# Kernel tuning notes

Hardware: AMD Instinct MI355X
Metric: run time of the kernel (lower is better)

Reference implementation:

```python
import jax, jax.numpy as jnp
import numpy as np

B, L, M = 32768, 128, 1024  # batch, latent_size, num_basis_function


def setup_inputs() -> dict:
    key = jax.random.key(0)
    k1, k2, k3 = jax.random.split(key, 3)
    u_lat = jax.random.normal(k1, (B, L), dtype=jnp.float32)
    centres = jax.random.normal(k2, (M, L), dtype=jnp.float32)      # RBF centres (torch init: N(0,1))
    log_sigmas = jnp.zeros((M,), dtype=jnp.float32)                  # RBF log bandwidths (torch init: 0)
    lin1_w = jax.random.normal(k3, (M,), dtype=jnp.float32) / np.float32(np.sqrt(M))  # Linear(M,1,bias=False)
    return {"u_lat": u_lat, "centres": centres, "log_sigmas": log_sigmas, "lin1_w": lin1_w}


def _V_batch(u, centres, log_sigmas, lin1_w):
    """Potential V(h) = ELU(w . multiquadric(||h-c||/sigma)) + 0.5*||h||^2, per row. Returns [B]."""
    u_sq = jnp.sum(u * u, axis=-1)                                   # [B]
    c_sq = jnp.sum(centres * centres, axis=-1)                       # [M]
    # ||h - c||^2 via norm expansion: avoids [B, M, L] intermediate
    sq_dist = jnp.maximum(u_sq[:, None] + c_sq[None, :] - 2.0 * (u @ centres.T), 0.0)  # [B, M]
    d = jnp.sqrt(sq_dist) / jnp.exp(log_sigmas)[None, :]             # [B, M]
    phi = jnp.sqrt(1.0 + d * d)                                      # multiquadric kernel
    e = jax.nn.elu(phi @ lin1_w)                                     # [B]
    return e + 0.5 * u_sq


def reference(u_lat, centres, log_sigmas, lin1_w):
    # LEBNN.forward: f_lat = dV/dh evaluated per sample (vmap(jacrev) in torch).
    # Each entry of _V_batch depends only on its own row of u_lat, so
    # grad of the summed potential gives the per-sample Jacobian rows exactly.
    grad_fn = jax.grad(lambda u: jnp.sum(_V_batch(u, centres, log_sigmas, lin1_w)))
    return grad_fn(u_lat)  # [B, L]
```

## Files before the change

### kernel.cpp

```cpp
#include <hip/hip_runtime.h>
#include <math.h>

#define B_N 32768
#define L_N 128
#define M_N 1024
#define NT 512
#define TB 64
#define TM 64
#define NCHUNK (M_N / TM)

typedef __bf16 v8bf __attribute__((ext_vector_type(8)));
typedef __bf16 v4bf __attribute__((ext_vector_type(4)));
typedef float  v4f  __attribute__((ext_vector_type(4)));

#define MFMA(a, b, c) __builtin_amdgcn_mfma_f32_16x16x32_bf16(a, b, c, 0, 0, 0)

#define US  136
#define CNS 136

__device__ inline v8bf pack8(float4 a, float4 b) {
    v8bf v;
    v[0] = (__bf16)a.x; v[1] = (__bf16)a.y; v[2] = (__bf16)a.z; v[3] = (__bf16)a.w;
    v[4] = (__bf16)b.x; v[5] = (__bf16)b.y; v[6] = (__bf16)b.z; v[7] = (__bf16)b.w;
    return v;
}

__global__ void lebnn_precompute(const float* __restrict__ centres,
                                 const float* __restrict__ log_sigmas,
                                 const float* __restrict__ lin_w,
                                 float4* __restrict__ cpack) {
    int m = blockIdx.x * blockDim.x + threadIdx.x;
    if (m >= M_N) return;
    const float4* row = (const float4*)(centres + (size_t)m * L_N);
    float s = 0.f;
#pragma unroll
    for (int i = 0; i < L_N / 4; ++i) {
        float4 v = row[i];
        s += v.x * v.x + v.y * v.y + v.z * v.z + v.w * v.w;
    }
    float4 p;
    p.x = s;
    p.y = expf(-2.f * log_sigmas[m]);
    p.z = lin_w[m];
    p.w = 0.f;
    cpack[m] = p;
}

__global__ void lebnn_transpose(const float* __restrict__ centres,
                                __bf16* __restrict__ cT) {
    __shared__ __bf16 tile[64 * 72];
    const int m0 = blockIdx.x * 64;
    const int l0 = blockIdx.y * 64;
    const int row = threadIdx.x >> 2;
    const int seg = threadIdx.x & 3;
    const float* src = centres + (size_t)(m0 + row) * L_N + l0 + seg * 16;
    float4 a0 = *(const float4*)(src);
    float4 a1 = *(const float4*)(src + 4);
    float4 a2 = *(const float4*)(src + 8);
    float4 a3 = *(const float4*)(src + 12);
    *(v8bf*)&tile[row * 72 + seg * 16]     = pack8(a0, a1);
    *(v8bf*)&tile[row * 72 + seg * 16 + 8] = pack8(a2, a3);
    __syncthreads();
    v8bf o0, o1;
#pragma unroll
    for (int i = 0; i < 8; ++i) o0[i] = tile[(seg * 16 + i) * 72 + row];
#pragma unroll
    for (int i = 0; i < 8; ++i) o1[i] = tile[(seg * 16 + 8 + i) * 72 + row];
    __bf16* dst = cT + (size_t)(l0 + row) * M_N + m0 + seg * 16;
    *(v8bf*)(dst)     = o0;
    *(v8bf*)(dst + 8) = o1;
}

__global__ __launch_bounds__(NT) void lebnn_phase1(
    const float* __restrict__ u, const float* __restrict__ centres,
    const float4* __restrict__ cpack, __bf16* __restrict__ qg,
    float* __restrict__ gg, float* __restrict__ rsg)
{
    __shared__ __bf16 u_bf[64 * US];
    __shared__ __bf16 c_n[64 * CNS];
    __shared__ float usq_s[64];
    __shared__ float upart[64 * 9];
    __shared__ float sred[288];
    __shared__ float rred[288];

    const int tid  = threadIdx.x;
    const int w    = tid >> 6;
    const int lane = tid & 63;
    const int l15  = lane & 15;
    const int l4   = lane >> 4;
    const int bh   = w >> 2;
    const int mq   = w & 3;
    const int b0   = blockIdx.x * TB;

    {
        int row = tid >> 3, seg = tid & 7;
        const float* up = u + (size_t)(b0 + row) * L_N + seg * 16;
        float4 a0 = *(const float4*)(up);
        float4 a1 = *(const float4*)(up + 4);
        float4 a2 = *(const float4*)(up + 8);
        float4 a3 = *(const float4*)(up + 12);
        float ps = a0.x*a0.x + a0.y*a0.y + a0.z*a0.z + a0.w*a0.w
                 + a1.x*a1.x + a1.y*a1.y + a1.z*a1.z + a1.w*a1.w
                 + a2.x*a2.x + a2.y*a2.y + a2.z*a2.z + a2.w*a2.w
                 + a3.x*a3.x + a3.y*a3.y + a3.z*a3.z + a3.w*a3.w;
        *(v8bf*)&u_bf[row * US + seg * 16]     = pack8(a0, a1);
        *(v8bf*)&u_bf[row * US + seg * 16 + 8] = pack8(a2, a3);
        upart[row * 9 + seg] = ps;
    }
    __syncthreads();
    if (tid < TB) {
        float s = 0.f;
#pragma unroll
        for (int i = 0; i < 8; ++i) s += upart[tid * 9 + i];
        usq_s[tid] = s;
    }
    __syncthreads();

    v8bf uf[2][4];
#pragma unroll
    for (int bt = 0; bt < 2; ++bt)
#pragma unroll
        for (int kk = 0; kk < 4; ++kk)
            uf[bt][kk] = *(v8bf*)&u_bf[(bh*32 + bt*16 + l15) * US + kk*32 + l4*8];

    float usq_r[2][4];
#pragma unroll
    for (int bt = 0; bt < 2; ++bt)
#pragma unroll
        for (int r = 0; r < 4; ++r)
            usq_r[bt][r] = usq_s[bh*32 + bt*16 + l4*4 + r];

    float s_p[2][4] = {{0.f,0.f,0.f,0.f},{0.f,0.f,0.f,0.f}};
    float r_p[2][4] = {{0.f,0.f,0.f,0.f},{0.f,0.f,0.f,0.f}};

    const int rp = tid >> 4;
    const int cg = tid & 15;

    for (int mt = 0; mt < NCHUNK; ++mt) {
        const int m0 = mt * TM;
        __syncthreads();
        {
            const float* cp0 = centres + (size_t)(m0 + 2*rp) * L_N + cg * 8;
            float4 r0a = *(const float4*)(cp0);
            float4 r0b = *(const float4*)(cp0 + 4);
            float4 r1a = *(const float4*)(cp0 + L_N);
            float4 r1b = *(const float4*)(cp0 + L_N + 4);
            *(v8bf*)&c_n[(2*rp)     * CNS + cg*8] = pack8(r0a, r0b);
            *(v8bf*)&c_n[(2*rp + 1) * CNS + cg*8] = pack8(r1a, r1b);
        }
        float4 cpv = cpack[m0 + mq*16 + l15];
        __syncthreads();

        v4f dot[2];
        dot[0] = (v4f){0.f,0.f,0.f,0.f};
        dot[1] = (v4f){0.f,0.f,0.f,0.f};
#pragma unroll
        for (int kk = 0; kk < 4; ++kk) {
            v8bf bfr = *(v8bf*)&c_n[(mq*16 + l15) * CNS + kk*32 + l4*8];
            dot[0] = MFMA(uf[0][kk], bfr, dot[0]);
            dot[1] = MFMA(uf[1][kk], bfr, dot[1]);
        }

        v8bf qv8;
        const float wq = cpv.z * cpv.y;
#pragma unroll
        for (int bt = 0; bt < 2; ++bt) {
#pragma unroll
            for (int r = 0; r < 4; ++r) {
                float dv  = dot[bt][r];
                float raw = fmaf(-2.f, dv, usq_r[bt][r] + cpv.x);
                float x   = fmaf(fmaxf(raw, 0.f), cpv.y, 1.f);
                float ri  = rsqrtf(x);
                s_p[bt][r] = fmaf(cpv.z, x * ri, s_p[bt][r]);
                float qv  = (raw > 0.f) ? wq * ri : 0.f;
                r_p[bt][r] += qv;
                qv8[bt*4 + r] = (__bf16)qv;
            }
        }
        *(v8bf*)(qg + ((size_t)blockIdx.x * NCHUNK + mt) * (NT * 8) + tid * 8) = qv8;
    }

#pragma unroll
    for (int bt = 0; bt < 2; ++bt)
#pragma unroll
        for (int r = 0; r < 4; ++r) {
#pragma unroll
            for (int msk = 1; msk < 16; msk <<= 1) {
                s_p[bt][r] += __shfl_xor(s_p[bt][r], msk, 64);
                r_p[bt][r] += __shfl_xor(r_p[bt][r], msk, 64);
            }
        }
    if (l15 == 0) {
#pragma unroll
        for (int bt = 0; bt < 2; ++bt)
#pragma unroll
            for (int r = 0; r < 4; ++r) {
                sred[w*36 + bt*16 + l4*4 + r] = s_p[bt][r];
                rred[w*36 + bt*16 + l4*4 + r] = r_p[bt][r];
            }
    }
    __syncthreads();

    if (tid < TB) {
        int bhh = tid >> 5, rowr = tid & 31;
        float s = 0.f, R = 0.f;
#pragma unroll
        for (int i = 0; i < 4; ++i) {
            s += sred[(bhh*4 + i)*36 + rowr];
            R += rred[(bhh*4 + i)*36 + rowr];
        }
        float g = (s > 0.f) ? 1.f : expf(s);
        gg[b0 + tid]  = g;
        rsg[b0 + tid] = fmaf(g, R, 1.f);
    }
}

__global__ __launch_bounds__(NT) void lebnn_gemm2(
    const float* __restrict__ u, const __bf16* __restrict__ qg,
    const __bf16* __restrict__ cT, const float* __restrict__ gg,
    const float* __restrict__ rsg, float* __restrict__ out)
{
    __shared__ __bf16 qt[64 * 72];
    __shared__ __bf16 ct[128 * 72];

    const int tid  = threadIdx.x;
    const int w    = tid >> 6;
    const int lane = tid & 63;
    const int l15  = lane & 15;
    const int l4   = lane >> 4;
    const int bh   = w >> 2;
    const int lq   = w & 3;
    const int bb0  = blockIdx.x * 64;

    v4f acc[2][2];
#pragma unroll
    for (int bt = 0; bt < 2; ++bt)
#pragma unroll
        for (int lt = 0; lt < 2; ++lt)
            acc[bt][lt] = (v4f){0.f, 0.f, 0.f, 0.f};

    for (int mt = 0; mt < NCHUNK; ++mt) {
        const int m0 = mt * TM;
        __syncthreads();
        {
            v8bf qv = *(const v8bf*)(qg + ((size_t)blockIdx.x * NCHUNK + mt) * (NT * 8) + tid * 8);
#pragma unroll
            for (int bt = 0; bt < 2; ++bt)
#pragma unroll
                for (int r = 0; r < 4; ++r)
                    qt[(bh*32 + bt*16 + l4*4 + r) * 72 + lq*16 + l15] = qv[bt*4 + r];
        }
        {
            int lr = tid >> 2, sg = tid & 3;
            const __bf16* src = cT + (size_t)lr * M_N + m0 + sg * 16;
            *(v8bf*)&ct[lr * 72 + sg * 16]     = *(const v8bf*)(src);
            *(v8bf*)&ct[lr * 72 + sg * 16 + 8] = *(const v8bf*)(src + 8);
        }
        __syncthreads();

#pragma unroll
        for (int kk = 0; kk < 2; ++kk) {
            v8bf qa0 = *(v8bf*)&qt[(bh*32 +  0 + l15) * 72 + kk*32 + l4*8];
            v8bf qa1 = *(v8bf*)&qt[(bh*32 + 16 + l15) * 72 + kk*32 + l4*8];
#pragma unroll
            for (int lt = 0; lt < 2; ++lt) {
                v8bf cb = *(v8bf*)&ct[(lq*32 + lt*16 + l15) * 72 + kk*32 + l4*8];
                acc[0][lt] = MFMA(qa0, cb, acc[0][lt]);
                acc[1][lt] = MFMA(qa1, cb, acc[1][lt]);
            }
        }
    }

    float gv[2][4], rv[2][4];
#pragma unroll
    for (int bt = 0; bt < 2; ++bt)
#pragma unroll
        for (int r = 0; r < 4; ++r) {
            int b = bb0 + bh*32 + bt*16 + l4*4 + r;
            gv[bt][r] = gg[b];
            rv[bt][r] = rsg[b];
        }
#pragma unroll
    for (int bt = 0; bt < 2; ++bt)
#pragma unroll
        for (int lt = 0; lt < 2; ++lt)
#pragma unroll
            for (int r = 0; r < 4; ++r) {
                size_t idx = (size_t)(bb0 + bh*32 + bt*16 + l4*4 + r) * L_N
                           + lq*32 + lt*16 + l15;
                out[idx] = fmaf(u[idx], rv[bt][r], -gv[bt][r] * acc[bt][lt][r]);
            }
}

#define CFS 68
#define OFF_UBF   0
#define OFF_CN    17408
#define OFF_CFL   34816
#define OFF_USQ   52224
#define OFF_UPART 52480
#define OFF_SRED  54784
#define OFF_RRED  55936
#define OFF_G     57088
#define OFF_RS    57344
#define SMEM_BYTES 57600

__global__ __launch_bounds__(NT) void lebnn_fallback(
    const float* __restrict__ u, const float* __restrict__ centres,
    const float4* __restrict__ cpack, float* __restrict__ out)
{
    extern __shared__ char smem[];
    __bf16* u_bf = (__bf16*)(smem + OFF_UBF);
    __bf16* c_n  = (__bf16*)(smem + OFF_CN);
    float*  cfl  = (float*)(smem + OFF_CFL);
    float* usq_s = (float*)(smem + OFF_USQ);
    float* upart = (float*)(smem + OFF_UPART);
    float* sred  = (float*)(smem + OFF_SRED);
    float* rred  = (float*)(smem + OFF_RRED);
    float* gsh   = (float*)(smem + OFF_G);
    float* rssh  = (float*)(smem + OFF_RS);

    const int tid  = threadIdx.x;
    const int w    = tid >> 6;
    const int lane = tid & 63;
    const int l15  = lane & 15;
    const int l4   = lane >> 4;
    const int bh   = w >> 2;
    const int mq   = w & 3;
    const int tx   = tid & 15;
    const int ty   = tid >> 4;
    const int b0   = blockIdx.x * TB;

    {
        int row = tid >> 3, seg = tid & 7;
        const float* up = u + (size_t)(b0 + row) * L_N + seg * 16;
        float4 a0 = *(const float4*)(up);
        float4 a1 = *(const float4*)(up + 4);
        float4 a2 = *(const float4*)(up + 8);
        float4 a3 = *(const float4*)(up + 12);
        float ps = a0.x*a0.x + a0.y*a0.y + a0.z*a0.z + a0.w*a0.w
                 + a1.x*a1.x + a1.y*a1.y + a1.z*a1.z + a1.w*a1.w
                 + a2.x*a2.x + a2.y*a2.y + a2.z*a2.z + a2.w*a2.w
                 + a3.x*a3.x + a3.y*a3.y + a3.z*a3.z + a3.w*a3.w;
        *(v8bf*)&u_bf[row * US + seg * 16]     = pack8(a0, a1);
        *(v8bf*)&u_bf[row * US + seg * 16 + 8] = pack8(a2, a3);
        upart[row * 9 + seg] = ps;
    }
    __syncthreads();
    if (tid < TB) {
        float s = 0.f;
#pragma unroll
        for (int i = 0; i < 8; ++i) s += upart[tid * 9 + i];
        usq_s[tid] = s;
    }
    __syncthreads();

    v8bf uf[2][4];
#pragma unroll
    for (int bt = 0; bt < 2; ++bt)
#pragma unroll
        for (int kk = 0; kk < 4; ++kk)
            uf[bt][kk] = *(v8bf*)&u_bf[(bh*32 + bt*16 + l15) * US + kk*32 + l4*8];

    float usq_r[2][4];
#pragma unroll
    for (int bt = 0; bt < 2; ++bt)
#pragma unroll
        for (int r = 0; r < 4; ++r)
            usq_r[bt][r] = usq_s[bh*32 + bt*16 + l4*4 + r];

    float s_p[2][4] = {{0.f,0.f,0.f,0.f},{0.f,0.f,0.f,0.f}};
    float r_p[2][4] = {{0.f,0.f,0.f,0.f},{0.f,0.f,0.f,0.f}};
    float T[4][4] = {{0.f}};

    const int rp = tid >> 4;
    const int cg = tid & 15;

    for (int mt = 0; mt < NCHUNK; ++mt) {
        const int m0 = mt * TM;
        __syncthreads();
        {
            const float* cp0 = centres + (size_t)(m0 + 2*rp) * L_N + cg * 8;
            float4 r0a = *(const float4*)(cp0);
            float4 r0b = *(const float4*)(cp0 + 4);
            float4 r1a = *(const float4*)(cp0 + L_N);
            float4 r1b = *(const float4*)(cp0 + L_N + 4);
            *(v8bf*)&c_n[(2*rp)     * CNS + cg*8] = pack8(r0a, r0b);
            *(v8bf*)&c_n[(2*rp + 1) * CNS + cg*8] = pack8(r1a, r1b);
        }
        float4 cpv = cpack[m0 + mq*16 + l15];
        __syncthreads();

        v4f dot[2];
        dot[0] = (v4f){0.f,0.f,0.f,0.f};
        dot[1] = (v4f){0.f,0.f,0.f,0.f};
#pragma unroll
        for (int kk = 0; kk < 4; ++kk) {
            v8bf bfr = *(v8bf*)&c_n[(mq*16 + l15) * CNS + kk*32 + l4*8];
            dot[0] = MFMA(uf[0][kk], bfr, dot[0]);
            dot[1] = MFMA(uf[1][kk], bfr, dot[1]);
        }

#pragma unroll
        for (int bt = 0; bt < 2; ++bt) {
#pragma unroll
            for (int r = 0; r < 4; ++r) {
                float dv  = dot[bt][r];
                float raw = fmaf(-2.f, dv, usq_r[bt][r] + cpv.x);
                float x   = fmaf(fmaxf(raw, 0.f), cpv.y, 1.f);
                float ri  = rsqrtf(x);
                s_p[bt][r] = fmaf(cpv.z, x * ri, s_p[bt][r]);
                float qv  = (raw > 0.f) ? cpv.z * cpv.y * ri : 0.f;
                r_p[bt][r] += qv;
                cfl[(mq*16 + l15) * CFS + bh*32 + bt*16 + l4*4 + r] = qv;
            }
        }
        __syncthreads();

        for (int mm = 0; mm < TM; ++mm) {
            v4f cf = *(v4f*)&cfl[mm * CFS + tx*4];
            v4bf cb = *(v4bf*)&c_n[mm * CNS + ty*4];
            float cv[4] = {(float)cb[0], (float)cb[1], (float)cb[2], (float)cb[3]};
#pragma unroll
            for (int i = 0; i < 4; ++i)
#pragma unroll
                for (int j = 0; j < 4; ++j)
                    T[i][j] = fmaf(cf[i], cv[j], T[i][j]);
        }
    }

    __syncthreads();

#pragma unroll
    for (int bt = 0; bt < 2; ++bt)
#pragma unroll
        for (int r = 0; r < 4; ++r) {
#pragma unroll
            for (int msk = 1; msk < 16; msk <<= 1) {
                s_p[bt][r] += __shfl_xor(s_p[bt][r], msk, 64);
                r_p[bt][r] += __shfl_xor(r_p[bt][r], msk, 64);
            }
        }
    if (l15 == 0) {
#pragma unroll
        for (int bt = 0; bt < 2; ++bt)
#pragma unroll
            for (int r = 0; r < 4; ++r) {
                sred[w*36 + bt*16 + l4*4 + r] = s_p[bt][r];
                rred[w*36 + bt*16 + l4*4 + r] = r_p[bt][r];
            }
    }
    __syncthreads();

    if (tid < TB) {
        int bhh = tid >> 5, rowr = tid & 31;
        float s = 0.f, R = 0.f;
#pragma unroll
        for (int i = 0; i < 4; ++i) {
            s += sred[(bhh*4 + i)*36 + rowr];
            R += rred[(bhh*4 + i)*36 + rowr];
        }
        float g = (s > 0.f) ? 1.f : expf(s);
        gsh[tid]  = g;
        rssh[tid] = fmaf(g, R, 1.f);
    }
    __syncthreads();

#pragma unroll
    for (int i = 0; i < 4; ++i) {
        int b = tx*4 + i;
        float rv = rssh[b];
        float gv = gsh[b];
        size_t idx = (size_t)(b0 + b) * L_N + ty*4;
        float4 uu = *(const float4*)(u + idx);
        float4 o;
        o.x = fmaf(uu.x, rv, -gv * T[i][0]);
        o.y = fmaf(uu.y, rv, -gv * T[i][1]);
        o.z = fmaf(uu.z, rv, -gv * T[i][2]);
        o.w = fmaf(uu.w, rv, -gv * T[i][3]);
        *(float4*)(out + idx) = o;
    }
}

extern "C" void kernel_launch(void* const* d_in, const int* in_sizes, int n_in,
                              void* d_out, int out_size, void* d_ws, size_t ws_size,
                              hipStream_t stream) {
    const float* u          = (const float*)d_in[0];
    const float* centres    = (const float*)d_in[1];
    const float* log_sigmas = (const float*)d_in[2];
    const float* lin_w      = (const float*)d_in[3];
    float* out = (float*)d_out;

    char* wsb = (char*)d_ws;
    float4* cpack = (float4*)wsb;
    __bf16* cT    = (__bf16*)(wsb + 16384);
    float*  gg    = (float*) (wsb + 278528);
    float*  rsg   = (float*) (wsb + 409600);
    __bf16* qg    = (__bf16*)(wsb + 540672);
    const size_t WS_NEED = 540672ULL + 67108864ULL;

    lebnn_precompute<<<(M_N + 255) / 256, 256, 0, stream>>>(centres, log_sigmas, lin_w, cpack);

    if (ws_size >= WS_NEED) {
        lebnn_transpose<<<dim3(M_N / 64, L_N / 64), 256, 0, stream>>>(centres, cT);
        lebnn_phase1<<<B_N / TB, NT, 0, stream>>>(u, centres, cpack, qg, gg, rsg);
        lebnn_gemm2<<<B_N / 64, NT, 0, stream>>>(u, qg, cT, gg, rsg, out);
    } else {
        hipFuncSetAttribute((const void*)lebnn_fallback,
                            hipFuncAttributeMaxDynamicSharedMemorySize, SMEM_BYTES);
        lebnn_fallback<<<B_N / TB, NT, SMEM_BYTES, stream>>>(u, centres, cpack, out);
    }
}
```

Measured before the change: 73.07 us.

## Pre-convert centres to bf16 once and prefetch gemm2 tiles into registers

The transpose kernel now also writes a row-major bf16 copy of the centres. Phase1 reads its MFMA B-fragments straight from global memory, which drops the per-chunk fp32 load, bf16 conversion, shared-memory staging and two barriers per chunk. Gemm2 software-prefetches the next chunk's q and cT data into registers while the current chunk computes. This costs extra workspace and relies on cache hits for the repeated global fragment reads in phase1.

Result: slower. 75.56 us (+3.4%).

```diff
diff --git a/kernel.cpp b/kernel.cpp
--- a/kernel.cpp
+++ b/kernel.cpp
@@ -47,7 +47,8 @@
 }
 
 __global__ void lebnn_transpose(const float* __restrict__ centres,
-                                __bf16* __restrict__ cT) {
+                                __bf16* __restrict__ cT,
+                                __bf16* __restrict__ cbn) {
     __shared__ __bf16 tile[64 * 72];
     const int m0 = blockIdx.x * 64;
     const int l0 = blockIdx.y * 64;
@@ -58,8 +59,13 @@
     float4 a1 = *(const float4*)(src + 4);
     float4 a2 = *(const float4*)(src + 8);
     float4 a3 = *(const float4*)(src + 12);
-    *(v8bf*)&tile[row * 72 + seg * 16]     = pack8(a0, a1);
-    *(v8bf*)&tile[row * 72 + seg * 16 + 8] = pack8(a2, a3);
+    v8bf p0 = pack8(a0, a1);
+    v8bf p1 = pack8(a2, a3);
+    *(v8bf*)&tile[row * 72 + seg * 16]     = p0;
+    *(v8bf*)&tile[row * 72 + seg * 16 + 8] = p1;
+    __bf16* rdst = cbn + (size_t)(m0 + row) * L_N + l0 + seg * 16;
+    *(v8bf*)(rdst)     = p0;
+    *(v8bf*)(rdst + 8) = p1;
     __syncthreads();
     v8bf o0, o1;
 #pragma unroll
@@ -72,12 +78,11 @@
 }
 
 __global__ __launch_bounds__(NT) void lebnn_phase1(
-    const float* __restrict__ u, const float* __restrict__ centres,
+    const float* __restrict__ u, const __bf16* __restrict__ cbn,
     const float4* __restrict__ cpack, __bf16* __restrict__ qg,
     float* __restrict__ gg, float* __restrict__ rsg)
 {
     __shared__ __bf16 u_bf[64 * US];
-    __shared__ __bf16 c_n[64 * CNS];
     __shared__ float usq_s[64];
     __shared__ float upart[64 * 9];
     __shared__ float sred[288];
@@ -133,30 +138,17 @@
     float s_p[2][4] = {{0.f,0.f,0.f,0.f},{0.f,0.f,0.f,0.f}};
     float r_p[2][4] = {{0.f,0.f,0.f,0.f},{0.f,0.f,0.f,0.f}};
 
-    const int rp = tid >> 4;
-    const int cg = tid & 15;
-
     for (int mt = 0; mt < NCHUNK; ++mt) {
         const int m0 = mt * TM;
-        __syncthreads();
-        {
-            const float* cp0 = centres + (size_t)(m0 + 2*rp) * L_N + cg * 8;
-            float4 r0a = *(const float4*)(cp0);
-            float4 r0b = *(const float4*)(cp0 + 4);
-            float4 r1a = *(const float4*)(cp0 + L_N);
-            float4 r1b = *(const float4*)(cp0 + L_N + 4);
-            *(v8bf*)&c_n[(2*rp)     * CNS + cg*8] = pack8(r0a, r0b);
-            *(v8bf*)&c_n[(2*rp + 1) * CNS + cg*8] = pack8(r1a, r1b);
-        }
         float4 cpv = cpack[m0 + mq*16 + l15];
-        __syncthreads();
+        const __bf16* bp = cbn + (size_t)(m0 + mq*16 + l15) * L_N + l4*8;
 
         v4f dot[2];
         dot[0] = (v4f){0.f,0.f,0.f,0.f};
         dot[1] = (v4f){0.f,0.f,0.f,0.f};
 #pragma unroll
         for (int kk = 0; kk < 4; ++kk) {
-            v8bf bfr = *(v8bf*)&c_n[(mq*16 + l15) * CNS + kk*32 + l4*8];
+            v8bf bfr = *(const v8bf*)(bp + kk*32);
             dot[0] = MFMA(uf[0][kk], bfr, dot[0]);
             dot[1] = MFMA(uf[1][kk], bfr, dot[1]);
         }
@@ -231,6 +223,8 @@
     const int bh   = w >> 2;
     const int lq   = w & 3;
     const int bb0  = blockIdx.x * 64;
+    const int lr   = tid >> 2;
+    const int sg   = tid & 3;
 
     v4f acc[2][2];
 #pragma unroll
@@ -239,24 +233,30 @@
         for (int lt = 0; lt < 2; ++lt)
             acc[bt][lt] = (v4f){0.f, 0.f, 0.f, 0.f};
 
+    v8bf qv  = *(const v8bf*)(qg + ((size_t)blockIdx.x * NCHUNK + 0) * (NT * 8) + tid * 8);
+    const __bf16* csrc = cT + (size_t)lr * M_N + sg * 16;
+    v8bf cva = *(const v8bf*)(csrc);
+    v8bf cvb = *(const v8bf*)(csrc + 8);
+
     for (int mt = 0; mt < NCHUNK; ++mt) {
-        const int m0 = mt * TM;
         __syncthreads();
         {
-            v8bf qv = *(const v8bf*)(qg + ((size_t)blockIdx.x * NCHUNK + mt) * (NT * 8) + tid * 8);
 #pragma unroll
             for (int bt = 0; bt < 2; ++bt)
 #pragma unroll
                 for (int r = 0; r < 4; ++r)
                     qt[(bh*32 + bt*16 + l4*4 + r) * 72 + lq*16 + l15] = qv[bt*4 + r];
-        }
-        {
-            int lr = tid >> 2, sg = tid & 3;
-            const __bf16* src = cT + (size_t)lr * M_N + m0 + sg * 16;
-            *(v8bf*)&ct[lr * 72 + sg * 16]     = *(const v8bf*)(src);
-            *(v8bf*)&ct[lr * 72 + sg * 16 + 8] = *(const v8bf*)(src + 8);
+            *(v8bf*)&ct[lr * 72 + sg * 16]     = cva;
+            *(v8bf*)&ct[lr * 72 + sg * 16 + 8] = cvb;
         }
         __syncthreads();
+
+        if (mt + 1 < NCHUNK) {
+            qv = *(const v8bf*)(qg + ((size_t)blockIdx.x * NCHUNK + (mt+1)) * (NT * 8) + tid * 8);
+            const __bf16* cn = cT + (size_t)lr * M_N + (mt+1) * TM + sg * 16;
+            cva = *(const v8bf*)(cn);
+            cvb = *(const v8bf*)(cn + 8);
+        }
 
 #pragma unroll
         for (int kk = 0; kk < 2; ++kk) {
@@ -493,16 +493,17 @@
     char* wsb = (char*)d_ws;
     float4* cpack = (float4*)wsb;
     __bf16* cT    = (__bf16*)(wsb + 16384);
-    float*  gg    = (float*) (wsb + 278528);
-    float*  rsg   = (float*) (wsb + 409600);
-    __bf16* qg    = (__bf16*)(wsb + 540672);
-    const size_t WS_NEED = 540672ULL + 67108864ULL;
+    __bf16* cbn   = (__bf16*)(wsb + 278528);
+    float*  gg    = (float*) (wsb + 540672);
+    float*  rsg   = (float*) (wsb + 671744);
+    __bf16* qg    = (__bf16*)(wsb + 802816);
+    const size_t WS_NEED = 802816ULL + 67108864ULL;
 
     lebnn_precompute<<<(M_N + 255) / 256, 256, 0, stream>>>(centres, log_sigmas, lin_w, cpack);
 
     if (ws_size >= WS_NEED) {
-        lebnn_transpose<<<dim3(M_N / 64, L_N / 64), 256, 0, stream>>>(centres, cT);
-        lebnn_phase1<<<B_N / TB, NT, 0, stream>>>(u, centres, cpack, qg, gg, rsg);
+        lebnn_transpose<<<dim3(M_N / 64, L_N / 64), 256, 0, stream>>>(centres, cT, cbn);
+        lebnn_phase1<<<B_N / TB, NT, 0, stream>>>(u, cbn, cpack, qg, gg, rsg);
         lebnn_gemm2<<<B_N / 64, NT, 0, stream>>>(u, qg, cT, gg, rsg, out);
     } else {
         hipFuncSetAttribute((const void*)lebnn_fallback,
```
